# Kernel optimization log

Measured on AMD Instinct MI355X. Metric: run time of the kernel, lower is better.

The kernel has to match this reference:

```python
import jax, jax.numpy as jnp
import numpy as np

B, CIN, T, H, W = 4, 3, 32, 64, 64
COUT = 64


def setup_inputs() -> dict:
    key = jax.random.key(0)
    ks = jax.random.split(key, 6)
    X = jax.random.normal(ks[0], (B, CIN, T, H, W), jnp.float32)
    # Conv3d weight (O, I, D, kH, kW) for kernel (2,3,3)
    Wconv = jax.random.normal(ks[1], (4 * COUT, CIN, 2, 3, 3), jnp.float32) * 0.1
    bconv = jax.random.normal(ks[2], (4 * COUT,), jnp.float32) * 0.1
    # QRNNCell peephole params, shape (out_channels, *frame_size)
    W_ci = jax.random.normal(ks[3], (COUT, H, W), jnp.float32) * 0.1
    W_cf = jax.random.normal(ks[4], (COUT, H, W), jnp.float32) * 0.1
    W_co = jax.random.normal(ks[5], (COUT, H, W), jnp.float32) * 0.1
    return {"X": X, "Wconv": Wconv, "bconv": bconv,
            "W_ci": W_ci, "W_cf": W_cf, "W_co": W_co}


def reference(X, Wconv, bconv, W_ci, W_cf, W_co):
    # ConstantPad3d((1,1,1,1,1,0)): W +-1, H +-1, time front +1
    Xp = jnp.pad(X, ((0, 0), (0, 0), (1, 0), (1, 1), (1, 1)))
    # Conv3d, kernel (2,3,3), VALID -> output (B, 4*COUT, T, H, W)
    E = jax.lax.conv_general_dilated(
        Xp, Wconv, window_strides=(1, 1, 1), padding='VALID',
        dimension_numbers=('NCDHW', 'OIDHW', 'NCDHW'))
    E = E + bconv[None, :, None, None, None]
    i_c, f_c, g_c, o_c = jnp.split(E, 4, axis=1)  # each (B, COUT, T, H, W)
    # time-major stacked gates: (T, 4, B, COUT, H, W)
    gates = jnp.stack([jnp.moveaxis(x, 2, 0) for x in (i_c, f_c, g_c, o_c)], axis=1)

    def step(carry, g4):
        Hs, Cs = carry
        i, f, g, o = g4[0], g4[1], g4[2], g4[3]
        ig = jax.nn.sigmoid(i + W_ci * Cs)
        fg = jax.nn.sigmoid(f + W_cf * Cs)
        Cn = fg * Cs + ig * jnp.tanh(g)
        og = jax.nn.sigmoid(o + W_co * Cn)
        Hn = og * jnp.tanh(Cn)
        return (Hn, Cn), Hn

    z = jnp.zeros((X.shape[0], W_ci.shape[0], X.shape[3], X.shape[4]), X.dtype)
    _, outs = jax.lax.scan(step, (z, z), gates)  # outs: (T, B, COUT, H, W)
    return jnp.moveaxis(outs, 0, 2)  # (B, COUT, T, H, W)
```

## Files before the change

### kernel.cpp

```cpp
#include <hip/hip_runtime.h>

#define TT     32
#define HW     4096
#define LROW   68
#define LPLANE (6 * LROW)
#define SXSZ   (3 * LPLANE)
#define NSTG   (3 * 6 * 66)

__device__ __forceinline__ float fsigmoid(float x) {
    return __builtin_amdgcn_rcpf(1.0f + __builtin_amdgcn_exp2f(x * -1.4426950408889634f));
}
__device__ __forceinline__ float ftanh(float x) {
    return 2.0f * __builtin_amdgcn_rcpf(1.0f + __builtin_amdgcn_exp2f(x * -2.8853900817779268f)) - 1.0f;
}
__device__ __forceinline__ float sgprf(float v) {
    return __uint_as_float(__builtin_amdgcn_readfirstlane(__float_as_uint(v)));
}

__global__ __launch_bounds__(256, 4) void convqrnn(
    const float* __restrict__ X,
    const float* __restrict__ Wc,
    const float* __restrict__ bc,
    const float* __restrict__ Wci,
    const float* __restrict__ Wcf,
    const float* __restrict__ Wco,
    float* __restrict__ out)
{
    __shared__ float sx[2 * SXSZ];
    __shared__ float gb[2 * 2048];

    const int tid = threadIdx.x;
    const int h0  = blockIdx.x * 4;
    const int co0 = blockIdx.y * 2;
    const int b   = blockIdx.z;

    const int g  = tid >> 6;
    const int l  = tid & 63;
    const int r  = l >> 4;
    const int c0 = (l & 15) * 4;

    const int prow = tid >> 6;
    const int pcol = tid & 63;
    const int opix = (h0 + prow) * 64 + pcol;

    const float wciA = Wci[co0 * HW + opix];
    const float wcfA = Wcf[co0 * HW + opix];
    const float wcoA = Wco[co0 * HW + opix];
    const float wciB = Wci[(co0 + 1) * HW + opix];
    const float wcfB = Wcf[(co0 + 1) * HW + opix];
    const float wcoB = Wco[(co0 + 1) * HW + opix];

    float wgtA[54], wgtB[54];
    {
        const float* __restrict__ wrA = Wc + (size_t)(g * 64 + co0) * 54;
        const float* __restrict__ wrB = wrA + 54;
        #pragma unroll
        for (int j = 0; j < 54; ++j) wgtA[j] = sgprf(wrA[j]);
        #pragma unroll
        for (int j = 0; j < 54; ++j) wgtB[j] = sgprf(wrB[j]);
    }
    const float bgA = sgprf(bc[g * 64 + co0]);
    const float bgB = sgprf(bc[g * 64 + co0 + 1]);

    const float* __restrict__ Xb = X + (size_t)b * (3 * TT * HW);
    int soff[5];
    int goff[5];
    int svmask = 0;
    #pragma unroll
    for (int k = 0; k < 5; ++k) {
        int idx  = tid + k * 256;
        bool inr = (idx < NSTG);
        int idc  = inr ? idx : 0;
        int ci   = idc / 396;
        int rem  = idc - ci * 396;
        int y    = rem / 66;
        int x    = rem - y * 66;
        int gh   = h0 + y - 1;
        int gw   = x - 1;
        bool v   = inr && (gh >= 0) && (gh < 64) && (gw >= 0) && (gw < 64);
        int ghc  = gh < 0 ? 0 : (gh > 63 ? 63 : gh);
        int gwc  = gw < 0 ? 0 : (gw > 63 ? 63 : gw);
        soff[k]  = inr ? (ci * LPLANE + y * LROW + x) : (LROW - 1);
        goff[k]  = ci * (TT * HW) + ghc * 64 + gwc;
        svmask  |= (v ? 1 : 0) << k;
    }

    #pragma unroll
    for (int k = 0; k < 5; ++k) {
        float v = ((svmask >> k) & 1) ? Xb[goff[k]] : 0.0f;
        sx[soff[k]] = v;
        goff[k] += HW;
    }

    float* __restrict__ outA = out + (size_t)(b * 64 + co0) * (TT * HW);
    float* __restrict__ outB = outA + (size_t)(TT * HW);
    int ooff = opix;

    float aA0 = 0.f, aA1 = 0.f, aA2 = 0.f, aA3 = 0.f;
    float aB0 = 0.f, aB1 = 0.f, aB2 = 0.f, aB3 = 0.f;
    float CA = 0.f, CB = 0.f;

    __syncthreads();

    for (int t = 0; t < TT; ++t) {
        const float* __restrict__ sxb = &sx[(t & 1) * SXSZ];
        float*       __restrict__ gbb = &gb[(t & 1) * 2048];

        float win[3][3][6];
        #pragma unroll
        for (int ci = 0; ci < 3; ++ci)
            #pragma unroll
            for (int kh = 0; kh < 3; ++kh) {
                const float* rowp = &sxb[ci * LPLANE + (r + kh) * LROW + c0];
                float4 lo = *(const float4*)rowp;
                float4 hi = *(const float4*)(rowp + 4);
                win[ci][kh][0] = lo.x; win[ci][kh][1] = lo.y;
                win[ci][kh][2] = lo.z; win[ci][kh][3] = lo.w;
                win[ci][kh][4] = hi.x; win[ci][kh][5] = hi.y;
            }

        float stv[5];
        if (t < TT - 1) {
            #pragma unroll
            for (int k = 0; k < 5; ++k) {
                stv[k] = ((svmask >> k) & 1) ? Xb[goff[k]] : 0.0f;
                goff[k] += HW;
            }
        }

        float sA0 = bgA, sA1 = bgA, sA2 = bgA, sA3 = bgA;
        float sB0 = bgB, sB1 = bgB, sB2 = bgB, sB3 = bgB;
        float nA0 = 0.f, nA1 = 0.f, nA2 = 0.f, nA3 = 0.f;
        float nB0 = 0.f, nB1 = 0.f, nB2 = 0.f, nB3 = 0.f;
        #pragma unroll
        for (int ci = 0; ci < 3; ++ci)
            #pragma unroll
            for (int kh = 0; kh < 3; ++kh)
                #pragma unroll
                for (int kw = 0; kw < 3; ++kw) {
                    const float w0 = win[ci][kh][kw + 0];
                    const float w1 = win[ci][kh][kw + 1];
                    const float w2 = win[ci][kh][kw + 2];
                    const float w3 = win[ci][kh][kw + 3];
                    const float wpA = wgtA[ci * 18 +     kh * 3 + kw];
                    const float wcA = wgtA[ci * 18 + 9 + kh * 3 + kw];
                    const float wpB = wgtB[ci * 18 +     kh * 3 + kw];
                    const float wcB = wgtB[ci * 18 + 9 + kh * 3 + kw];
                    sA0 += wcA * w0;  sA1 += wcA * w1;
                    sA2 += wcA * w2;  sA3 += wcA * w3;
                    nA0 += wpA * w0;  nA1 += wpA * w1;
                    nA2 += wpA * w2;  nA3 += wpA * w3;
                    sB0 += wcB * w0;  sB1 += wcB * w1;
                    sB2 += wcB * w2;  sB3 += wcB * w3;
                    nB0 += wpB * w0;  nB1 += wpB * w1;
                    nB2 += wpB * w2;  nB3 += wpB * w3;
                }

        float4 gvA = make_float4(sA0 + aA0, sA1 + aA1, sA2 + aA2, sA3 + aA3);
        float4 gvB = make_float4(sB0 + aB0, sB1 + aB1, sB2 + aB2, sB3 + aB3);
        aA0 = nA0; aA1 = nA1; aA2 = nA2; aA3 = nA3;
        aB0 = nB0; aB1 = nB1; aB2 = nB2; aB3 = nB3;
        *(float4*)&gbb[g * 256 + r * 64 + c0]        = gvA;
        *(float4*)&gbb[1024 + g * 256 + r * 64 + c0] = gvB;

        if (t < TT - 1) {
            float* __restrict__ sxn = &sx[((t + 1) & 1) * SXSZ];
            #pragma unroll
            for (int k = 0; k < 5; ++k) sxn[soff[k]] = stv[k];
        }

        __syncthreads();

        {
            const float iv = gbb[tid];
            const float fv = gbb[256 + tid];
            const float gg = gbb[512 + tid];
            const float ov = gbb[768 + tid];
            const float ig = fsigmoid(iv + wciA * CA);
            const float fg = fsigmoid(fv + wcfA * CA);
            const float Cn = fg * CA + ig * ftanh(gg);
            const float og = fsigmoid(ov + wcoA * Cn);
            outA[ooff] = og * ftanh(Cn);
            CA = Cn;
        }
        {
            const float iv = gbb[1024 + tid];
            const float fv = gbb[1024 + 256 + tid];
            const float gg = gbb[1024 + 512 + tid];
            const float ov = gbb[1024 + 768 + tid];
            const float ig = fsigmoid(iv + wciB * CB);
            const float fg = fsigmoid(fv + wcfB * CB);
            const float Cn = fg * CB + ig * ftanh(gg);
            const float og = fsigmoid(ov + wcoB * Cn);
            outB[ooff] = og * ftanh(Cn);
            CB = Cn;
        }
        ooff += HW;
    }
}

extern "C" void kernel_launch(void* const* d_in, const int* in_sizes, int n_in,
                              void* d_out, int out_size, void* d_ws, size_t ws_size,
                              hipStream_t stream) {
    const float* X   = (const float*)d_in[0];
    const float* Wc  = (const float*)d_in[1];
    const float* bc  = (const float*)d_in[2];
    const float* Wci = (const float*)d_in[3];
    const float* Wcf = (const float*)d_in[4];
    const float* Wco = (const float*)d_in[5];
    float* out = (float*)d_out;

    dim3 grid(16, 32, 4);
    convqrnn<<<grid, 256, 0, stream>>>(X, Wc, bc, Wci, Wcf, Wco, out);
}
```

Baseline: 438.7 us.

## Stage conv weights in LDS with broadcast float4 reads instead of SGPRs

Moves the per-block convolution weights from 108 scalar registers into a packed shared-memory table read with broadcast float4 loads each timestep. The input window is loaded per (ci,kh) row inside the FMA loop rather than all up front, and a never-true store keeps the compiler from hoisting the weight loads. This targets SGPR pressure and live-register count, at the cost of extra LDS traffic per step. The launch bound minimum occupancy is lowered from 4 to 2 blocks.

```diff
diff --git a/kernel.cpp b/kernel.cpp
--- a/kernel.cpp
+++ b/kernel.cpp
@@ -17,7 +17,7 @@
     return __uint_as_float(__builtin_amdgcn_readfirstlane(__float_as_uint(v)));
 }
 
-__global__ __launch_bounds__(256, 4) void convqrnn(
+__global__ __launch_bounds__(256, 2) void convqrnn(
     const float* __restrict__ X,
     const float* __restrict__ Wc,
     const float* __restrict__ bc,
@@ -28,6 +28,7 @@
 {
     __shared__ float sx[2 * SXSZ];
     __shared__ float gb[2 * 2048];
+    __shared__ float wl[576];
 
     const int tid = threadIdx.x;
     const int h0  = blockIdx.x * 4;
@@ -50,14 +51,19 @@
     const float wcfB = Wcf[(co0 + 1) * HW + opix];
     const float wcoB = Wco[(co0 + 1) * HW + opix];
 
-    float wgtA[54], wgtB[54];
-    {
-        const float* __restrict__ wrA = Wc + (size_t)(g * 64 + co0) * 54;
-        const float* __restrict__ wrB = wrA + 54;
-        #pragma unroll
-        for (int j = 0; j < 54; ++j) wgtA[j] = sgprf(wrA[j]);
-        #pragma unroll
-        for (int j = 0; j < 54; ++j) wgtB[j] = sgprf(wrB[j]);
+    for (int fi = tid; fi < 432; fi += 256) {
+        int grp   = fi / 12;
+        int e     = fi - grp * 12;
+        int g2    = grp / 9;
+        int ck    = grp - g2 * 9;
+        int ci    = ck / 3;
+        int kh    = ck - ci * 3;
+        int which = e / 3;
+        int kw    = e - which * 3;
+        int cs    = which >> 1;
+        int dt    = which & 1;
+        wl[grp * 16 + e] =
+            Wc[(size_t)(g2 * 64 + co0 + cs) * 54 + ci * 18 + dt * 9 + kh * 3 + kw];
     }
     const float bgA = sgprf(bc[g * 64 + co0]);
     const float bgB = sgprf(bc[g * 64 + co0 + 1]);
@@ -103,21 +109,10 @@
     __syncthreads();
 
     for (int t = 0; t < TT; ++t) {
+        if (blockIdx.x == 0xFFFFFFFFu) wl[tid] = 0.0f;
+
         const float* __restrict__ sxb = &sx[(t & 1) * SXSZ];
         float*       __restrict__ gbb = &gb[(t & 1) * 2048];
-
-        float win[3][3][6];
-        #pragma unroll
-        for (int ci = 0; ci < 3; ++ci)
-            #pragma unroll
-            for (int kh = 0; kh < 3; ++kh) {
-                const float* rowp = &sxb[ci * LPLANE + (r + kh) * LROW + c0];
-                float4 lo = *(const float4*)rowp;
-                float4 hi = *(const float4*)(rowp + 4);
-                win[ci][kh][0] = lo.x; win[ci][kh][1] = lo.y;
-                win[ci][kh][2] = lo.z; win[ci][kh][3] = lo.w;
-                win[ci][kh][4] = hi.x; win[ci][kh][5] = hi.y;
-            }
 
         float stv[5];
         if (t < TT - 1) {
@@ -135,26 +130,34 @@
         #pragma unroll
         for (int ci = 0; ci < 3; ++ci)
             #pragma unroll
-            for (int kh = 0; kh < 3; ++kh)
-                #pragma unroll
-                for (int kw = 0; kw < 3; ++kw) {
-                    const float w0 = win[ci][kh][kw + 0];
-                    const float w1 = win[ci][kh][kw + 1];
-                    const float w2 = win[ci][kh][kw + 2];
-                    const float w3 = win[ci][kh][kw + 3];
-                    const float wpA = wgtA[ci * 18 +     kh * 3 + kw];
-                    const float wcA = wgtA[ci * 18 + 9 + kh * 3 + kw];
-                    const float wpB = wgtB[ci * 18 +     kh * 3 + kw];
-                    const float wcB = wgtB[ci * 18 + 9 + kh * 3 + kw];
-                    sA0 += wcA * w0;  sA1 += wcA * w1;
-                    sA2 += wcA * w2;  sA3 += wcA * w3;
-                    nA0 += wpA * w0;  nA1 += wpA * w1;
-                    nA2 += wpA * w2;  nA3 += wpA * w3;
-                    sB0 += wcB * w0;  sB1 += wcB * w1;
-                    sB2 += wcB * w2;  sB3 += wcB * w3;
-                    nB0 += wpB * w0;  nB1 += wpB * w1;
-                    nB2 += wpB * w2;  nB3 += wpB * w3;
-                }
+            for (int kh = 0; kh < 3; ++kh) {
+                const float* rowp = &sxb[ci * LPLANE + (r + kh) * LROW + c0];
+                float4 lo = *(const float4*)rowp;
+                float2 hi = *(const float2*)(rowp + 4);
+                const float w0 = lo.x, w1 = lo.y, w2 = lo.z;
+                const float w3 = lo.w, w4 = hi.x, w5 = hi.y;
+
+                const int ws = (g * 9 + ci * 3 + kh) * 16;
+                float4 qa = *(const float4*)&wl[ws];
+                float4 qb = *(const float4*)&wl[ws + 4];
+                float4 qc = *(const float4*)&wl[ws + 8];
+
+                sA0 += qa.w * w0;  sA1 += qa.w * w1;  sA2 += qa.w * w2;  sA3 += qa.w * w3;
+                sA0 += qb.x * w1;  sA1 += qb.x * w2;  sA2 += qb.x * w3;  sA3 += qb.x * w4;
+                sA0 += qb.y * w2;  sA1 += qb.y * w3;  sA2 += qb.y * w4;  sA3 += qb.y * w5;
+
+                nA0 += qa.x * w0;  nA1 += qa.x * w1;  nA2 += qa.x * w2;  nA3 += qa.x * w3;
+                nA0 += qa.y * w1;  nA1 += qa.y * w2;  nA2 += qa.y * w3;  nA3 += qa.y * w4;
+                nA0 += qa.z * w2;  nA1 += qa.z * w3;  nA2 += qa.z * w4;  nA3 += qa.z * w5;
+
+                sB0 += qc.y * w0;  sB1 += qc.y * w1;  sB2 += qc.y * w2;  sB3 += qc.y * w3;
+                sB0 += qc.z * w1;  sB1 += qc.z * w2;  sB2 += qc.z * w3;  sB3 += qc.z * w4;
+                sB0 += qc.w * w2;  sB1 += qc.w * w3;  sB2 += qc.w * w4;  sB3 += qc.w * w5;
+
+                nB0 += qb.z * w0;  nB1 += qb.z * w1;  nB2 += qb.z * w2;  nB3 += qb.z * w3;
+                nB0 += qb.w * w1;  nB1 += qb.w * w2;  nB2 += qb.w * w3;  nB3 += qb.w * w4;
+                nB0 += qc.x * w2;  nB1 += qc.x * w3;  nB2 += qc.x * w4;  nB3 += qc.x * w5;
+            }
 
         float4 gvA = make_float4(sA0 + aA0, sA1 + aA1, sA2 + aA2, sA3 + aA3);
         float4 gvB = make_float4(sB0 + aB0, sB1 + aB1, sB2 + aB2, sB3 + aB3);
```

New measurement: 377.5 us. -13.9%, faster.
